# Optimization experiments

Hardware: AMD Instinct MI355X
Metric: run time of the kernel (lower is better)

The kernel has to match this reference:

```python
import jax, jax.numpy as jnp
import numpy as np

NUM_MARGINALS = 8
NUM_NODES = 128
BOX_LOWER = -4.0
BOX_UPPER = 4.0


def _coefficients(nodal_values):
    # Natural cubic spline coefficients per marginal.
    n = NUM_NODES
    h = (BOX_UPPER - BOX_LOWER) / (n - 1)  # uniform step size
    diag = jnp.ones(n, dtype=nodal_values.dtype).at[1:-1].set(4.0)
    sup = jnp.ones(n - 1, dtype=nodal_values.dtype).at[0].set(0.0)
    sub = jnp.ones(n - 1, dtype=nodal_values.dtype).at[-1].set(0.0)
    A = jnp.diag(diag) + jnp.diag(sup, 1) + jnp.diag(sub, -1)  # (n, n) tridiagonal
    rhs = jnp.zeros((NUM_MARGINALS, n), dtype=nodal_values.dtype)
    rhs = rhs.at[:, 1:-1].set(
        3.0 * (nodal_values[:, :-2] - 2.0 * nodal_values[:, 1:-1] + nodal_values[:, 2:]) / (h * h)
    )
    c = jnp.linalg.solve(A, rhs.T).T                      # (f, n)  2nd-order coeffs
    b = (nodal_values[:, 1:] - nodal_values[:, :-1]) / h - h * (2.0 * c[:, :-1] + c[:, 1:]) / 3.0  # (f, n-1)
    d = (c[:, 1:] - c[:, :-1]) / (3.0 * h)                # (f, n-1)
    return nodal_values, b, c, d


def reference(x, nodal_values):
    n = NUM_NODES
    bs, f, w, h_sp = x.shape
    nodes = jnp.linspace(BOX_LOWER, BOX_UPPER, n, dtype=x.dtype)
    # bucketise: clamp(ceil(scaled * (n-1)) - 1, 0, n-2)
    x_scaled = (x - BOX_LOWER) / (BOX_UPPER - BOX_LOWER)
    idx = jnp.clip(jnp.ceil(x_scaled * (n - 1)).astype(jnp.int32) - 1, 0, n - 2)  # (bs,f,w,h)
    y = x - nodes[idx]
    a_t, b_t, c_t, d_t = _coefficients(nodal_values)
    idx_f = jnp.transpose(idx, (1, 0, 2, 3)).reshape(f, -1)  # (f, bs*w*h)

    def gather(coeff):
        g = jnp.take_along_axis(coeff, idx_f, axis=1)
        return jnp.transpose(g.reshape(f, bs, w, h_sp), (1, 0, 2, 3))

    a = gather(a_t)
    b = gather(b_t)
    c = gather(c_t)
    d = gather(d_t)
    # cubic Horner evaluation + global sum
    return jnp.sum(a + y * (b + y * (c + y * d)))


def setup_inputs() -> dict:
    key = jax.random.key(0)
    k1, k2 = jax.random.split(key)
    x = jax.random.normal(k1, (32, 8, 256, 256), dtype=jnp.float32)
    nodal_values = jax.random.normal(k2, (NUM_MARGINALS, NUM_NODES), dtype=jnp.float32)
    return {"x": x, "nodal_values": nodal_values}
```

## Files before the change

### kernel.cpp

```cpp
#include <hip/hip_runtime.h>

#define NM 8
#define NN 128
#define NI 127
#define SPAD 129

#define GRID 2048
#define PT 8

struct CpTab { float v[NN]; };
constexpr CpTab make_cp() {
    CpTab t{};
    t.v[0] = 0.0f;
    double p = 0.0;
    for (int i = 1; i <= 126; ++i) { p = 1.0 / (4.0 - p); t.v[i] = (float)p; }
    t.v[127] = 0.0f;
    return t;
}
__constant__ CpTab CP = make_cp();

__device__ __forceinline__ float eval1(float xv,
                                       const float2* __restrict__ tAB,
                                       const float2* __restrict__ tCD) {
    float t = xv + 4.0f;
    int idx = (int)ceilf(t * 15.875f) - 1;
    idx = min(max(idx, 0), NI - 1);
    float y = fmaf((float)idx, -(8.0f / 127.0f), t);
    float2 ab = tAB[idx];
    float2 cd = tCD[idx];
    return fmaf(y, fmaf(y, fmaf(y, cd.y, cd.x), ab.y), ab.x);
}

__global__ __launch_bounds__(256)
void spline_fused_kernel(const float4* __restrict__ x,
                         const float* __restrict__ nodal,
                         float* __restrict__ partials, int n4) {
    __shared__ float  yv[NM * NN];
    __shared__ float  sc[NM * SPAD];
    __shared__ float2 tabAB[NM * NI];
    __shared__ float2 tabCD[NM * NI];
    __shared__ float  wsum[4];

    const int tid = threadIdx.x;
    const float h      = 8.0f / 127.0f;
    const float inv_h  = 127.0f / 8.0f;
    const float inv_h2 = inv_h * inv_h;

    for (int t = tid; t < NM * NN; t += 256) yv[t] = nodal[t];
    __syncthreads();
    for (int t = tid; t < NM * 126; t += 256) {
        int f = t / 126, i = t - f * 126 + 1;
        sc[f * SPAD + i] = 3.0f * (yv[f * NN + i - 1] - 2.0f * yv[f * NN + i]
                                   + yv[f * NN + i + 1]) * inv_h2;
    }
    __syncthreads();

    if (tid < NM) {
        const int f = tid;
        float prev = 0.0f;
        #pragma unroll
        for (int i = 1; i <= 126; ++i) {
            prev = (sc[f * SPAD + i] - prev) * CP.v[i];
            sc[f * SPAD + i] = prev;
        }
        float cn = 0.0f;
        #pragma unroll
        for (int i = 126; i >= 1; --i) {
            cn = sc[f * SPAD + i] - CP.v[i] * cn;
            sc[f * SPAD + i] = cn;
        }
        sc[f * SPAD + 0]   = 0.0f;
        sc[f * SPAD + 127] = 0.0f;
    }
    __syncthreads();

    for (int t = tid; t < NM * NI; t += 256) {
        int f = t / NI, i = t - f * NI;
        float ci  = sc[f * SPAD + i];
        float ci1 = sc[f * SPAD + i + 1];
        float a = yv[f * NN + i];
        float b = (yv[f * NN + i + 1] - a) * inv_h - h * (2.0f * ci + ci1) * (1.0f / 3.0f);
        float d = (ci1 - ci) * inv_h * (1.0f / 3.0f);
        tabAB[t] = make_float2(a, b);
        tabCD[t] = make_float2(ci, d);
    }
    __syncthreads();

    const int gid = blockIdx.x * 256 + tid;
    const int S   = GRID * 256;
    const int f = (gid >> 14) & 7;
    const float2* __restrict__ tAB = tabAB + f * NI;
    const float2* __restrict__ tCD = tabCD + f * NI;

    float acc = 0.0f;
    if (gid + (PT - 1) * S < n4) {
        float4 v[PT];
        #pragma unroll
        for (int k = 0; k < PT; ++k) v[k] = x[gid + k * S];
        #pragma unroll
        for (int k = 0; k < PT; ++k) {
            acc += eval1(v[k].x, tAB, tCD);
            acc += eval1(v[k].y, tAB, tCD);
            acc += eval1(v[k].z, tAB, tCD);
            acc += eval1(v[k].w, tAB, tCD);
        }
    } else {
        for (int k = 0; k < PT; ++k) {
            int i = gid + k * S;
            if (i < n4) {
                float4 v = x[i];
                acc += eval1(v.x, tAB, tCD); acc += eval1(v.y, tAB, tCD);
                acc += eval1(v.z, tAB, tCD); acc += eval1(v.w, tAB, tCD);
            }
        }
    }

    #pragma unroll
    for (int off = 32; off > 0; off >>= 1) acc += __shfl_down(acc, off);
    int lane = tid & 63;
    int wid  = tid >> 6;
    if (lane == 0) wsum[wid] = acc;
    __syncthreads();
    if (tid == 0) partials[blockIdx.x] = wsum[0] + wsum[1] + wsum[2] + wsum[3];
}

__global__ __launch_bounds__(256)
void final_reduce_kernel(const float* __restrict__ partials, float* __restrict__ out) {
    __shared__ float wsum[4];
    float a = 0.0f;
    for (int i = threadIdx.x; i < GRID; i += 256) a += partials[i];
    #pragma unroll
    for (int off = 32; off > 0; off >>= 1) a += __shfl_down(a, off);
    int lane = threadIdx.x & 63, wid = threadIdx.x >> 6;
    if (lane == 0) wsum[wid] = a;
    __syncthreads();
    if (threadIdx.x == 0) out[0] = wsum[0] + wsum[1] + wsum[2] + wsum[3];
}

extern "C" void kernel_launch(void* const* d_in, const int* in_sizes, int n_in,
                              void* d_out, int out_size, void* d_ws, size_t ws_size,
                              hipStream_t stream) {
    const float* x     = (const float*)d_in[0];
    const float* nodal = (const float*)d_in[1];
    float* out      = (float*)d_out;
    float* partials = (float*)d_ws;

    int n4 = in_sizes[0] / 4;
    spline_fused_kernel<<<GRID, 256, 0, stream>>>((const float4*)x, nodal, partials, n4);
    final_reduce_kernel<<<1, 256, 0, stream>>>(partials, out);
}
```

Before: 114.5 us.

## Replace serial tridiagonal solve with banded inverse-weight convolution and prefetch x loads

After: 102.8 us. 1.11x faster.

```diff
diff --git a/kernel.cpp b/kernel.cpp
--- a/kernel.cpp
+++ b/kernel.cpp
@@ -3,21 +3,38 @@
 #define NM 8
 #define NN 128
 #define NI 127
-#define SPAD 129
 
 #define GRID 2048
 #define PT 8
 
-struct CpTab { float v[NN]; };
-constexpr CpTab make_cp() {
-    CpTab t{};
-    t.v[0] = 0.0f;
-    double p = 0.0;
-    for (int i = 1; i <= 126; ++i) { p = 1.0 / (4.0 - p); t.v[i] = (float)p; }
-    t.v[127] = 0.0f;
+struct WTab { float v[33 * 128]; };
+constexpr WTab make_wt() {
+    WTab t{};
+    double cp[NI];
+    cp[0] = 0.0;
+    for (int i = 1; i <= 126; ++i) cp[i] = 1.0 / (4.0 - cp[i - 1]);
+    for (int i0 = 1; i0 <= 126; ++i0) {
+        double dp[NN] = {};
+        double prev = 0.0;
+        for (int i = 1; i <= 126; ++i) {
+            double rhs = (i == i0) ? 1.0 : 0.0;
+            prev = (rhs - prev) * cp[i];
+            dp[i] = prev;
+        }
+        double w[NN] = {};
+        double cn = 0.0;
+        for (int i = 126; i >= 1; --i) {
+            cn = dp[i] - cp[i] * cn;
+            w[i] = cn;
+        }
+        for (int k = 0; k < 33; ++k) {
+            int j = i0 - 16 + k;
+            if (j >= 1 && j <= 126) t.v[k * 128 + i0] = (float)w[j];
+        }
+    }
     return t;
 }
-__constant__ CpTab CP = make_cp();
+__constant__ WTab WT = make_wt();
 
 __device__ __forceinline__ float eval1(float xv,
                                        const float2* __restrict__ tAB,
@@ -35,68 +52,74 @@
 void spline_fused_kernel(const float4* __restrict__ x,
                          const float* __restrict__ nodal,
                          float* __restrict__ partials, int n4) {
-    __shared__ float  yv[NM * NN];
-    __shared__ float  sc[NM * SPAD];
+    __shared__ float  rhsPad[NM][160];
+    __shared__ float  sc[NM][NN];
     __shared__ float2 tabAB[NM * NI];
     __shared__ float2 tabCD[NM * NI];
     __shared__ float  wsum[4];
 
     const int tid = threadIdx.x;
-    const float h      = 8.0f / 127.0f;
-    const float inv_h  = 127.0f / 8.0f;
-    const float inv_h2 = inv_h * inv_h;
+    const int gid = blockIdx.x * 256 + tid;
+    const int S   = GRID * 256;
 
-    for (int t = tid; t < NM * NN; t += 256) yv[t] = nodal[t];
-    __syncthreads();
-    for (int t = tid; t < NM * 126; t += 256) {
-        int f = t / 126, i = t - f * 126 + 1;
-        sc[f * SPAD + i] = 3.0f * (yv[f * NN + i - 1] - 2.0f * yv[f * NN + i]
-                                   + yv[f * NN + i + 1]) * inv_h2;
+    float4 v[PT];
+    bool full = (gid + (PT - 1) * S < n4);
+    if (full) {
+        #pragma unroll
+        for (int k = 0; k < PT; ++k) v[k] = x[gid + k * S];
+    }
+
+    const float inv_h2 = (127.0f / 8.0f) * (127.0f / 8.0f);
+    #pragma unroll
+    for (int u = 0; u < 5; ++u) {
+        int t = tid + u * 256;
+        int f = t / 160, j = t - f * 160;
+        int jc = j - 16;
+        float val = 0.0f;
+        if (jc >= 1 && jc <= 126)
+            val = 3.0f * (nodal[f * NN + jc - 1] - 2.0f * nodal[f * NN + jc]
+                          + nodal[f * NN + jc + 1]) * inv_h2;
+        rhsPad[f][j] = val;
     }
     __syncthreads();
 
-    if (tid < NM) {
-        const int f = tid;
-        float prev = 0.0f;
-        #pragma unroll
-        for (int i = 1; i <= 126; ++i) {
-            prev = (sc[f * SPAD + i] - prev) * CP.v[i];
-            sc[f * SPAD + i] = prev;
+    {
+        const int i = tid & 127;
+        const int g = tid >> 7;
+        float a0 = 0.f, a1 = 0.f, a2 = 0.f, a3 = 0.f;
+        for (int k = 0; k < 33; ++k) {
+            float w = WT.v[k * 128 + i];
+            a0 = fmaf(w, rhsPad[g    ][i + k], a0);
+            a1 = fmaf(w, rhsPad[g + 2][i + k], a1);
+            a2 = fmaf(w, rhsPad[g + 4][i + k], a2);
+            a3 = fmaf(w, rhsPad[g + 6][i + k], a3);
         }
-        float cn = 0.0f;
-        #pragma unroll
-        for (int i = 126; i >= 1; --i) {
-            cn = sc[f * SPAD + i] - CP.v[i] * cn;
-            sc[f * SPAD + i] = cn;
-        }
-        sc[f * SPAD + 0]   = 0.0f;
-        sc[f * SPAD + 127] = 0.0f;
+        sc[g    ][i] = a0;
+        sc[g + 2][i] = a1;
+        sc[g + 4][i] = a2;
+        sc[g + 6][i] = a3;
     }
     __syncthreads();
 
+    const float h = 8.0f / 127.0f, inv_h = 127.0f / 8.0f;
     for (int t = tid; t < NM * NI; t += 256) {
         int f = t / NI, i = t - f * NI;
-        float ci  = sc[f * SPAD + i];
-        float ci1 = sc[f * SPAD + i + 1];
-        float a = yv[f * NN + i];
-        float b = (yv[f * NN + i + 1] - a) * inv_h - h * (2.0f * ci + ci1) * (1.0f / 3.0f);
+        float ci  = sc[f][i];
+        float ci1 = sc[f][i + 1];
+        float a = nodal[f * NN + i];
+        float b = (nodal[f * NN + i + 1] - a) * inv_h - h * (2.0f * ci + ci1) * (1.0f / 3.0f);
         float d = (ci1 - ci) * inv_h * (1.0f / 3.0f);
         tabAB[t] = make_float2(a, b);
         tabCD[t] = make_float2(ci, d);
     }
     __syncthreads();
 
-    const int gid = blockIdx.x * 256 + tid;
-    const int S   = GRID * 256;
     const int f = (gid >> 14) & 7;
     const float2* __restrict__ tAB = tabAB + f * NI;
     const float2* __restrict__ tCD = tabCD + f * NI;
 
     float acc = 0.0f;
-    if (gid + (PT - 1) * S < n4) {
-        float4 v[PT];
-        #pragma unroll
-        for (int k = 0; k < PT; ++k) v[k] = x[gid + k * S];
+    if (full) {
         #pragma unroll
         for (int k = 0; k < PT; ++k) {
             acc += eval1(v[k].x, tAB, tCD);
@@ -108,9 +131,9 @@
         for (int k = 0; k < PT; ++k) {
             int i = gid + k * S;
             if (i < n4) {
-                float4 v = x[i];
-                acc += eval1(v.x, tAB, tCD); acc += eval1(v.y, tAB, tCD);
-                acc += eval1(v.z, tAB, tCD); acc += eval1(v.w, tAB, tCD);
+                float4 vv = x[i];
+                acc += eval1(vv.x, tAB, tCD); acc += eval1(vv.y, tAB, tCD);
+                acc += eval1(vv.z, tAB, tCD); acc += eval1(vv.w, tAB, tCD);
             }
         }
     }
@@ -146,6 +169,7 @@
     float* partials = (float*)d_ws;
 
     int n4 = in_sizes[0] / 4;
+
     spline_fused_kernel<<<GRID, 256, 0, stream>>>((const float4*)x, nodal, partials, n4);
     final_reduce_kernel<<<1, 256, 0, stream>>>(partials, out);
 }
```
